# Kernel tuning notes

Measured on AMD Instinct MI355X. Metric: run time of the kernel, lower is better.

Reference implementation:

```python
import jax, jax.numpy as jnp
import numpy as np

HEAD_SIZE = 64


def setup_inputs() -> dict:
    key = jax.random.key(0)
    k1, k2, k3, k4 = jax.random.split(key, 4)
    B, T, C = 4, 4096, 1024
    x = jax.random.normal(k1, (B, T, C), dtype=jnp.float32)
    s = 1.0 / np.sqrt(C)  # ~kaiming-uniform scale for Linear weights
    Wk = jax.random.normal(k2, (C, HEAD_SIZE), dtype=jnp.float32) * s
    Wq = jax.random.normal(k3, (C, HEAD_SIZE), dtype=jnp.float32) * s
    Wv = jax.random.normal(k4, (C, HEAD_SIZE), dtype=jnp.float32) * s
    return {"x": x, "Wk": Wk, "Wq": Wq, "Wv": Wv}


def reference(x, Wk, Wq, Wv):
    # x: [B,T,C]; Wk/Wq/Wv: [C,H]
    B, T, C = x.shape
    H = Wk.shape[1]
    k = jnp.einsum('btc,ch->bth', x, Wk)
    q = jnp.einsum('btc,ch->bth', x, Wq)
    v = jnp.einsum('btc,ch->bth', x, Wv)
    scale = 1.0 / jnp.sqrt(jnp.asarray(H, dtype=x.dtype))
    scores = jnp.einsum('bqh,bkh->bqk', q, k) * scale  # [B,T,T]
    causal = jnp.tril(jnp.ones((T, T), dtype=bool))
    scores = jnp.where(causal, scores, jnp.asarray(-jnp.inf, dtype=scores.dtype))
    attn = jax.nn.softmax(scores, axis=-1)
    out = jnp.einsum('bqk,bkh->bqh', attn, v)  # [B,T,H]
    return out
```

## Files before the change

kernel.cpp:

```cpp
#include <hip/hip_runtime.h>
#include <hip/hip_bf16.h>

#define T_ 4096
#define C_ 1024
#define H_ 64
#define LSTR 72
#define XSTR 132

typedef short bf16x8 __attribute__((ext_vector_type(8)));
typedef float f32x4 __attribute__((ext_vector_type(4)));

__device__ __forceinline__ short f2bf(float f) {
  union { __hip_bfloat16 h; short s; } u;
  u.h = __float2bfloat16(f);
  return u.s;
}
__device__ __forceinline__ unsigned pack2(float a, float b) {
  return ((unsigned)(unsigned short)f2bf(b) << 16) | (unsigned short)f2bf(a);
}

__global__ void wtrans_kernel(const float* __restrict__ Wk,
                              const float* __restrict__ Wq,
                              const float* __restrict__ Wv,
                              __hip_bfloat16* __restrict__ Wt) {
  int tid = blockIdx.x * 256 + threadIdx.x;
  if (tid >= 192 * 1024) return;
  int n = tid >> 10;
  int c = tid & 1023;
  const float* W = (n < 64) ? Wk : ((n < 128) ? Wq : Wv);
  Wt[tid] = __float2bfloat16(W[c * 64 + (n & 63)]);
}

__global__ __launch_bounds__(256) void proj_kernel(
    const float* __restrict__ x, const __hip_bfloat16* __restrict__ Wt,
    __hip_bfloat16* __restrict__ qb, __hip_bfloat16* __restrict__ Kf,
    __hip_bfloat16* __restrict__ Vf) {
  __shared__ float Xl[2][16 * XSTR];
  const int tid = threadIdx.x;
  const int lane = tid & 63;
  const int wave = tid >> 6;
  const int m = lane & 15;
  const int quad = lane >> 4;
  const int rt = blockIdx.x;
  const int t0 = rt * 16;

  const float* xbase = x + (size_t)t0 * C_;

  if (wave == 3) {
#pragma unroll
    for (int i = 0; i < 8; ++i) {
      const int linear = i * 64 + lane;
      const int row = linear >> 5;
      const int c4 = linear & 31;
      float4 v = *(const float4*)(xbase + (size_t)row * C_ + c4 * 4);
      *(float4*)&Xl[0][row * XSTR + c4 * 4] = v;
    }
  }
  __syncthreads();

  f32x4 acc[4];
#pragma unroll
  for (int i = 0; i < 4; ++i) acc[i] = (f32x4){0.f, 0.f, 0.f, 0.f};

  const int which = wave;
  const __hip_bfloat16* wrow = Wt + ((size_t)which * 64 + m) * C_ + quad * 8;

  for (int c = 0; c < 8; ++c) {
    if (wave == 3) {
      if (c + 1 < 8) {
        const float* src = xbase + (c + 1) * 128;
        float* dst = &Xl[(c + 1) & 1][0];
#pragma unroll
        for (int i = 0; i < 8; ++i) {
          const int linear = i * 64 + lane;
          const int row = linear >> 5;
          const int c4 = linear & 31;
          float4 v = *(const float4*)(src + (size_t)row * C_ + c4 * 4);
          *(float4*)&dst[row * XSTR + c4 * 4] = v;
        }
      }
    } else {
      bf16x8 bq[16];
#pragma unroll
      for (int ks = 0; ks < 4; ++ks)
#pragma unroll
        for (int nt = 0; nt < 4; ++nt)
          bq[ks * 4 + nt] =
              *(const bf16x8*)(wrow + (size_t)nt * 16 * C_ + c * 128 + ks * 32);
      const float* xl = &Xl[c & 1][m * XSTR + quad * 8];
#pragma unroll
      for (int ks = 0; ks < 4; ++ks) {
        float4 xa = *(const float4*)(xl + ks * 32);
        float4 xb = *(const float4*)(xl + ks * 32 + 4);
        bf16x8 a;
        a[0] = f2bf(xa.x); a[1] = f2bf(xa.y); a[2] = f2bf(xa.z); a[3] = f2bf(xa.w);
        a[4] = f2bf(xb.x); a[5] = f2bf(xb.y); a[6] = f2bf(xb.z); a[7] = f2bf(xb.w);
#pragma unroll
        for (int nt = 0; nt < 4; ++nt)
          acc[nt] = __builtin_amdgcn_mfma_f32_16x16x32_bf16(a, bq[ks * 4 + nt],
                                                            acc[nt], 0, 0, 0);
      }
    }
    __syncthreads();
  }

  const int bb = t0 >> 12;
  const int tloc = t0 & (T_ - 1);
  const int ktile = tloc >> 6;

  if (which == 1) {
    const float cscale = 0.18033688011112042f;
#pragma unroll
    for (int nt = 0; nt < 4; ++nt)
#pragma unroll
      for (int r = 0; r < 4; ++r)
        qb[(size_t)(t0 + quad * 4 + r) * H_ + nt * 16 + m] =
            __float2bfloat16(acc[nt][r] * cscale);
  } else if (which == 0) {
    __hip_bfloat16* dst = Kf + ((size_t)bb * 64 + ktile) * 4096;
    const int ntK = (tloc >> 4) & 3;
#pragma unroll
    for (int nt = 0; nt < 4; ++nt) {
      const int wh = nt >> 1;
      const int quadK = (nt * 2 + (m >> 3)) & 3;
      const int j = m & 7;
#pragma unroll
      for (int r = 0; r < 4; ++r) {
        const int mK = quad * 4 + r;
        dst[(ntK * 2 + wh) * 512 + (quadK * 16 + mK) * 8 + j] = __float2bfloat16(acc[nt][r]);
      }
    }
  } else if (which == 2) {
    __hip_bfloat16* dst = Vf + ((size_t)bb * 64 + ktile) * 4096;
#pragma unroll
    for (int nt = 0; nt < 4; ++nt) {
#pragma unroll
      for (int r = 0; r < 4; ++r) {
        const int kvo = (tloc & 63) + quad * 4 + r;
        const int half = (kvo >> 5) & 1;
        const int quadV = (kvo >> 3) & 3;
        const int j = kvo & 7;
        dst[(nt * 2 + half) * 512 + (quadV * 16 + m) * 8 + j] = __float2bfloat16(acc[nt][r]);
      }
    }
  }
}

__global__ __launch_bounds__(256, 4) void fa_pass1(
    const __hip_bfloat16* __restrict__ qg, const __hip_bfloat16* __restrict__ Kf,
    const __hip_bfloat16* __restrict__ Vf, float* __restrict__ Opart,
    float* __restrict__ Ml) {
  __shared__ __hip_bfloat16 Pl[4][16 * LSTR];
  const int lane = threadIdx.x & 63;
  const int wave = threadIdx.x >> 6;
  const int m = lane & 15;
  const int quad = lane >> 4;

  const int jid = blockIdx.x * 4 + wave;
  const int b = jid / 1152;
  const int j2 = jid - b * 1152;
  int g = 7;
  while (16 * g * (g + 1) > j2) --g;
  const int r2 = j2 - 16 * g * (g + 1);
  const int qt = 32 * g + r2 / (g + 1);
  const int c = r2 - (r2 / (g + 1)) * (g + 1);
  const int q0 = qt * 16;
  const int k0s = c * 512;
  const int kend0 = k0s + 512;
  const int kend = (kend0 < q0 + 16) ? kend0 : (q0 + 16);
  const int ntile = (kend - k0s + 63) >> 6;

  const __hip_bfloat16* qbase = qg + ((size_t)b * T_ + q0 + m) * H_;
  bf16x8 qf0 = *(const bf16x8*)(qbase + quad * 8);
  bf16x8 qf1 = *(const bf16x8*)(qbase + 32 + quad * 8);

  f32x4 Oacc[4];
#pragma unroll
  for (int i = 0; i < 4; ++i) Oacc[i] = (f32x4){0.f, 0.f, 0.f, 0.f};
  float psum = 0.f;

  const __hip_bfloat16* kgf = Kf + (size_t)b * 262144 + lane * 8;
  const __hip_bfloat16* vgf = Vf + (size_t)b * 262144 + lane * 8;
  __hip_bfloat16* Plw = &Pl[wave][0];

  for (int it = 0; it < ntile; ++it) {
    const int ktile = (k0s >> 6) + it;
    const int k0 = ktile * 64;
    const __hip_bfloat16* kp = kgf + (size_t)ktile * 4096;
    const __hip_bfloat16* vp = vgf + (size_t)ktile * 4096;

    f32x4 s[4];
#pragma unroll
    for (int nt = 0; nt < 4; ++nt) {
      bf16x8 kf0 = *(const bf16x8*)(kp + nt * 1024);
      bf16x8 kf1 = *(const bf16x8*)(kp + nt * 1024 + 512);
      f32x4 t = (f32x4){0.f, 0.f, 0.f, 0.f};
      t = __builtin_amdgcn_mfma_f32_16x16x32_bf16(kf0, qf0, t, 0, 0, 0);
      t = __builtin_amdgcn_mfma_f32_16x16x32_bf16(kf1, qf1, t, 0, 0, 0);
      s[nt] = t;
    }
    bf16x8 vf[8];
#pragma unroll
    for (int nt = 0; nt < 4; ++nt) {
      vf[2 * nt] = *(const bf16x8*)(vp + nt * 1024);
      vf[2 * nt + 1] = *(const bf16x8*)(vp + nt * 1024 + 512);
    }

    const bool needmask = (k0 + 63 > q0);
#pragma unroll
    for (int nt = 0; nt < 4; ++nt) {
      float p[4];
#pragma unroll
      for (int r = 0; r < 4; ++r) {
        float sv = s[nt][r];
        if (needmask && (k0 + nt * 16 + quad * 4 + r) > (q0 + m))
          sv = -__builtin_inff();
        p[r] = exp2f(sv);
        psum += p[r];
      }
      uint2 u = {pack2(p[0], p[1]), pack2(p[2], p[3])};
      *(uint2*)(&Plw[m * LSTR + nt * 16 + quad * 4]) = u;
    }

    bf16x8 pf0 = *(const bf16x8*)(&Plw[m * LSTR + quad * 8]);
    bf16x8 pf1 = *(const bf16x8*)(&Plw[m * LSTR + 32 + quad * 8]);
#pragma unroll
    for (int nt = 0; nt < 4; ++nt) {
      Oacc[nt] = __builtin_amdgcn_mfma_f32_16x16x32_bf16(pf0, vf[2 * nt], Oacc[nt], 0, 0, 0);
      Oacc[nt] = __builtin_amdgcn_mfma_f32_16x16x32_bf16(pf1, vf[2 * nt + 1], Oacc[nt], 0, 0, 0);
    }
  }

  psum += __shfl_xor(psum, 16);
  psum += __shfl_xor(psum, 32);

  float* Op = Opart + (size_t)jid * 1024;
#pragma unroll
  for (int nt = 0; nt < 4; ++nt)
#pragma unroll
    for (int r = 0; r < 4; ++r)
      Op[(quad * 4 + r) * 64 + nt * 16 + m] = Oacc[nt][r];
  if (lane < 16) Ml[(size_t)jid * 16 + lane] = psum;
}

__global__ __launch_bounds__(256) void fa_combine(
    const float* __restrict__ Opart, const float* __restrict__ Ml,
    float* __restrict__ out) {
  const int bq = blockIdx.x;
  const int b = bq >> 8;
  const int qt = bq & 255;
  const int g = qt >> 5;
  const int nc = g + 1;
  const int jbase = b * 1152 + 16 * g * (g + 1) + (qt & 31) * nc;
  const int r = threadIdx.x >> 4;
  const int h0 = (threadIdx.x & 15) * 4;

  float4 O = {0.f, 0.f, 0.f, 0.f};
  float L = 0.f;
  for (int c = 0; c < nc; ++c) {
    L += Ml[(size_t)(jbase + c) * 16 + r];
    float4 o = *(const float4*)(Opart + (size_t)(jbase + c) * 1024 + r * 64 + h0);
    O.x += o.x; O.y += o.y; O.z += o.z; O.w += o.w;
  }
  float inv = 1.f / L;
  float4 res = {O.x * inv, O.y * inv, O.z * inv, O.w * inv};
  *(float4*)(out + ((size_t)b * T_ + qt * 16 + r) * H_ + h0) = res;
}

extern "C" void kernel_launch(void* const* d_in, const int* in_sizes, int n_in,
                              void* d_out, int out_size, void* d_ws, size_t ws_size,
                              hipStream_t stream) {
  const float* x = (const float*)d_in[0];
  const float* Wk = (const float*)d_in[1];
  const float* Wq = (const float*)d_in[2];
  const float* Wv = (const float*)d_in[3];
  float* out = (float*)d_out;
  char* ws = (char*)d_ws;
  __hip_bfloat16* Wt = (__hip_bfloat16*)ws;
  __hip_bfloat16* qb = (__hip_bfloat16*)(ws + 393216);
  __hip_bfloat16* Kf = (__hip_bfloat16*)(ws + 2490368);
  __hip_bfloat16* Vf = (__hip_bfloat16*)(ws + 4587520);
  float* Opart = (float*)(ws + 6684672);
  float* Ml = (float*)(ws + 25559040);

  hipLaunchKernelGGL(wtrans_kernel, dim3(768), dim3(256), 0, stream, Wk, Wq, Wv, Wt);
  hipLaunchKernelGGL(proj_kernel, dim3(1024), dim3(256), 0, stream, x, Wt, qb, Kf, Vf);
  hipLaunchKernelGGL(fa_pass1, dim3(1152), dim3(256), 0, stream, qb, Kf, Vf, Opart, Ml);
  hipLaunchKernelGGL(fa_combine, dim3(1024), dim3(256), 0, stream, Opart, Ml, out);
}
```

Measured before the change: 172.6 us.

## Restructure QKV projection: full-tile bf16 LDS staging, fragment-ordered weights, all waves compute

The weight pre-pass now writes W directly in MFMA B-fragment order, so each lane loads its fragment with one contiguous 16-byte read. The projection kernel loads the whole 16x1024 x tile at once, converts it to bf16 while storing it to LDS, and drops the double-buffered loop with its per-chunk barriers. The 12 output 16-column tiles are split three per wave across all four waves, where previously one wave only loaded data. The cost is a larger up-front load with no overlap against compute, plus more registers held for the 16 float4 values per thread.

```diff
diff --git a/kernel.cpp b/kernel.cpp
--- a/kernel.cpp
+++ b/kernel.cpp
@@ -5,7 +5,7 @@
 #define C_ 1024
 #define H_ 64
 #define LSTR 72
-#define XSTR 132
+#define XBS 1032
 
 typedef short bf16x8 __attribute__((ext_vector_type(8)));
 typedef float f32x4 __attribute__((ext_vector_type(4)));
@@ -22,125 +22,116 @@
 __global__ void wtrans_kernel(const float* __restrict__ Wk,
                               const float* __restrict__ Wq,
                               const float* __restrict__ Wv,
-                              __hip_bfloat16* __restrict__ Wt) {
+                              __hip_bfloat16* __restrict__ Wtf) {
   int tid = blockIdx.x * 256 + threadIdx.x;
-  if (tid >= 192 * 1024) return;
-  int n = tid >> 10;
-  int c = tid & 1023;
-  const float* W = (n < 64) ? Wk : ((n < 128) ? Wq : Wv);
-  Wt[tid] = __float2bfloat16(W[c * 64 + (n & 63)]);
+  const int j = tid & 7;
+  const int lane = (tid >> 3) & 63;
+  const int m = lane & 15;
+  const int quad = lane >> 4;
+  const int f = (tid >> 9) & 15;
+  const int nt = f & 3;
+  const int ks = f >> 2;
+  const int c = (tid >> 13) & 7;
+  const int which = tid >> 16;
+  const float* W = (which == 0) ? Wk : ((which == 1) ? Wq : Wv);
+  const int cc = c * 128 + ks * 32 + quad * 8 + j;
+  const int h = nt * 16 + m;
+  Wtf[tid] = __float2bfloat16(W[cc * 64 + h]);
 }
 
 __global__ __launch_bounds__(256) void proj_kernel(
-    const float* __restrict__ x, const __hip_bfloat16* __restrict__ Wt,
+    const float* __restrict__ x, const __hip_bfloat16* __restrict__ Wtf,
     __hip_bfloat16* __restrict__ qb, __hip_bfloat16* __restrict__ Kf,
     __hip_bfloat16* __restrict__ Vf) {
-  __shared__ float Xl[2][16 * XSTR];
+  __shared__ __hip_bfloat16 Xb[16 * XBS];
   const int tid = threadIdx.x;
   const int lane = tid & 63;
   const int wave = tid >> 6;
   const int m = lane & 15;
   const int quad = lane >> 4;
-  const int rt = blockIdx.x;
-  const int t0 = rt * 16;
-
-  const float* xbase = x + (size_t)t0 * C_;
-
-  if (wave == 3) {
-#pragma unroll
-    for (int i = 0; i < 8; ++i) {
-      const int linear = i * 64 + lane;
-      const int row = linear >> 5;
-      const int c4 = linear & 31;
-      float4 v = *(const float4*)(xbase + (size_t)row * C_ + c4 * 4);
-      *(float4*)&Xl[0][row * XSTR + c4 * 4] = v;
-    }
+  const int t0 = blockIdx.x * 16;
+
+  const float4* xtile = (const float4*)(x + (size_t)t0 * C_);
+  float4 xv[16];
+#pragma unroll
+  for (int k = 0; k < 16; ++k) xv[k] = xtile[tid + k * 256];
+#pragma unroll
+  for (int k = 0; k < 16; ++k) {
+    const int idx = tid + k * 256;
+    const int row = idx >> 8;
+    const int c4 = idx & 255;
+    uint2 u = {pack2(xv[k].x, xv[k].y), pack2(xv[k].z, xv[k].w)};
+    *(uint2*)(&Xb[row * XBS + c4 * 4]) = u;
   }
   __syncthreads();
 
-  f32x4 acc[4];
-#pragma unroll
-  for (int i = 0; i < 4; ++i) acc[i] = (f32x4){0.f, 0.f, 0.f, 0.f};
-
-  const int which = wave;
-  const __hip_bfloat16* wrow = Wt + ((size_t)which * 64 + m) * C_ + quad * 8;
-
+  int whichs[3], ntls[3];
+  const __hip_bfloat16* wb[3];
+#pragma unroll
+  for (int i = 0; i < 3; ++i) {
+    const int g = wave * 3 + i;
+    whichs[i] = g >> 2;
+    ntls[i] = g & 3;
+    wb[i] = Wtf + (size_t)whichs[i] * 65536 + ntls[i] * 512 + lane * 8;
+  }
+  f32x4 acc[3];
+#pragma unroll
+  for (int i = 0; i < 3; ++i) acc[i] = (f32x4){0.f, 0.f, 0.f, 0.f};
+
+#pragma unroll
   for (int c = 0; c < 8; ++c) {
-    if (wave == 3) {
-      if (c + 1 < 8) {
-        const float* src = xbase + (c + 1) * 128;
-        float* dst = &Xl[(c + 1) & 1][0];
-#pragma unroll
-        for (int i = 0; i < 8; ++i) {
-          const int linear = i * 64 + lane;
-          const int row = linear >> 5;
-          const int c4 = linear & 31;
-          float4 v = *(const float4*)(src + (size_t)row * C_ + c4 * 4);
-          *(float4*)&dst[row * XSTR + c4 * 4] = v;
-        }
-      }
-    } else {
-      bf16x8 bq[16];
+    bf16x8 bq[12];
+#pragma unroll
+    for (int i = 0; i < 3; ++i)
 #pragma unroll
       for (int ks = 0; ks < 4; ++ks)
-#pragma unroll
-        for (int nt = 0; nt < 4; ++nt)
-          bq[ks * 4 + nt] =
-              *(const bf16x8*)(wrow + (size_t)nt * 16 * C_ + c * 128 + ks * 32);
-      const float* xl = &Xl[c & 1][m * XSTR + quad * 8];
-#pragma unroll
-      for (int ks = 0; ks < 4; ++ks) {
-        float4 xa = *(const float4*)(xl + ks * 32);
-        float4 xb = *(const float4*)(xl + ks * 32 + 4);
-        bf16x8 a;
-        a[0] = f2bf(xa.x); a[1] = f2bf(xa.y); a[2] = f2bf(xa.z); a[3] = f2bf(xa.w);
-        a[4] = f2bf(xb.x); a[5] = f2bf(xb.y); a[6] = f2bf(xb.z); a[7] = f2bf(xb.w);
-#pragma unroll
-        for (int nt = 0; nt < 4; ++nt)
-          acc[nt] = __builtin_amdgcn_mfma_f32_16x16x32_bf16(a, bq[ks * 4 + nt],
-                                                            acc[nt], 0, 0, 0);
-      }
-    }
-    __syncthreads();
+        bq[i * 4 + ks] = *(const bf16x8*)(wb[i] + (c * 16 + ks * 4) * 512);
+#pragma unroll
+    for (int ks = 0; ks < 4; ++ks) {
+      bf16x8 a = *(const bf16x8*)(&Xb[m * XBS + c * 128 + ks * 32 + quad * 8]);
+#pragma unroll
+      for (int i = 0; i < 3; ++i)
+        acc[i] = __builtin_amdgcn_mfma_f32_16x16x32_bf16(a, bq[i * 4 + ks],
+                                                         acc[i], 0, 0, 0);
+    }
   }
 
   const int bb = t0 >> 12;
   const int tloc = t0 & (T_ - 1);
   const int ktile = tloc >> 6;
-
-  if (which == 1) {
-    const float cscale = 0.18033688011112042f;
-#pragma unroll
-    for (int nt = 0; nt < 4; ++nt)
+  const float cscale = 0.18033688011112042f;
+
+#pragma unroll
+  for (int i = 0; i < 3; ++i) {
+    const int which = whichs[i];
+    const int ntl = ntls[i];
+    if (which == 1) {
 #pragma unroll
       for (int r = 0; r < 4; ++r)
-        qb[(size_t)(t0 + quad * 4 + r) * H_ + nt * 16 + m] =
-            __float2bfloat16(acc[nt][r] * cscale);
-  } else if (which == 0) {
-    __hip_bfloat16* dst = Kf + ((size_t)bb * 64 + ktile) * 4096;
-    const int ntK = (tloc >> 4) & 3;
-#pragma unroll
-    for (int nt = 0; nt < 4; ++nt) {
-      const int wh = nt >> 1;
-      const int quadK = (nt * 2 + (m >> 3)) & 3;
+        qb[(size_t)(t0 + quad * 4 + r) * H_ + ntl * 16 + m] =
+            __float2bfloat16(acc[i][r] * cscale);
+    } else if (which == 0) {
+      __hip_bfloat16* dst = Kf + ((size_t)bb * 64 + ktile) * 4096;
+      const int ntK = (tloc >> 4) & 3;
+      const int wh = ntl >> 1;
+      const int quadK = (ntl * 2 + (m >> 3)) & 3;
       const int j = m & 7;
 #pragma unroll
       for (int r = 0; r < 4; ++r) {
         const int mK = quad * 4 + r;
-        dst[(ntK * 2 + wh) * 512 + (quadK * 16 + mK) * 8 + j] = __float2bfloat16(acc[nt][r]);
+        dst[(ntK * 2 + wh) * 512 + (quadK * 16 + mK) * 8 + j] =
+            __float2bfloat16(acc[i][r]);
       }
-    }
-  } else if (which == 2) {
-    __hip_bfloat16* dst = Vf + ((size_t)bb * 64 + ktile) * 4096;
-#pragma unroll
-    for (int nt = 0; nt < 4; ++nt) {
+    } else {
+      __hip_bfloat16* dst = Vf + ((size_t)bb * 64 + ktile) * 4096;
 #pragma unroll
       for (int r = 0; r < 4; ++r) {
         const int kvo = (tloc & 63) + quad * 4 + r;
         const int half = (kvo >> 5) & 1;
         const int quadV = (kvo >> 3) & 3;
         const int j = kvo & 7;
-        dst[(nt * 2 + half) * 512 + (quadV * 16 + m) * 8 + j] = __float2bfloat16(acc[nt][r]);
+        dst[(ntl * 2 + half) * 512 + (quadV * 16 + m) * 8 + j] =
+            __float2bfloat16(acc[i][r]);
       }
     }
   }
@@ -276,15 +267,15 @@
   const float* Wv = (const float*)d_in[3];
   float* out = (float*)d_out;
   char* ws = (char*)d_ws;
-  __hip_bfloat16* Wt = (__hip_bfloat16*)ws;
+  __hip_bfloat16* Wtf = (__hip_bfloat16*)ws;
   __hip_bfloat16* qb = (__hip_bfloat16*)(ws + 393216);
   __hip_bfloat16* Kf = (__hip_bfloat16*)(ws + 2490368);
   __hip_bfloat16* Vf = (__hip_bfloat16*)(ws + 4587520);
   float* Opart = (float*)(ws + 6684672);
   float* Ml = (float*)(ws + 25559040);
 
-  hipLaunchKernelGGL(wtrans_kernel, dim3(768), dim3(256), 0, stream, Wk, Wq, Wv, Wt);
-  hipLaunchKernelGGL(proj_kernel, dim3(1024), dim3(256), 0, stream, x, Wt, qb, Kf, Vf);
+  hipLaunchKernelGGL(wtrans_kernel, dim3(768), dim3(256), 0, stream, Wk, Wq, Wv, Wtf);
+  hipLaunchKernelGGL(proj_kernel, dim3(1024), dim3(256), 0, stream, x, Wtf, qb, Kf, Vf);
   hipLaunchKernelGGL(fa_pass1, dim3(1152), dim3(256), 0, stream, qb, Kf, Vf, Opart, Ml);
   hipLaunchKernelGGL(fa_combine, dim3(1024), dim3(256), 0, stream, Opart, Ml, out);
 }
```

New measurement: 144.9 us. 16.0% less time.
